# Performance work log

Hardware: AMD Instinct MI355X
Metric: run time of the kernel (lower is better)

Reference implementation:

```python
import jax, jax.numpy as jnp
import numpy as np


def setup_inputs() -> dict:
    key = jax.random.key(0)
    k1, k2 = jax.random.split(key)
    B, D, N = 8, 3, 8192
    preds = jax.random.normal(k1, (B, D, N), dtype=jnp.float32)
    gts = jax.random.normal(k2, (B, D, N), dtype=jnp.float32)
    return {"preds": preds, "gts": gts}


def _chamfer(preds, gts):
    # preds, gts: [B, 3, N] -> x, y: [B, N, 3]
    x = jnp.swapaxes(preds, 2, 1)
    y = jnp.swapaxes(gts, 2, 1)
    # Squared-norm rows/cols + cross term: P[b,i,j] = |x_i|^2 + |y_j|^2 - 2 x_i.y_j
    rx = jnp.sum(x * x, axis=-1)              # [B, Nx]
    ry = jnp.sum(y * y, axis=-1)              # [B, Ny]
    zz = jnp.einsum("bnd,bmd->bnm", x, y)     # [B, Nx, Ny]
    P = rx[:, :, None] + ry[:, None, :] - 2.0 * zz
    loss_1 = jnp.sum(jnp.min(P, axis=1))      # nearest pred for each gt
    loss_2 = jnp.sum(jnp.min(P, axis=2))      # nearest gt for each pred
    return loss_1 + loss_2


def reference(preds, gts):
    return _chamfer(preds, gts)
```

## Files before the change

kernel.cpp:

```cpp
#include <hip/hip_runtime.h>
#include <hip/hip_bf16.h>


typedef float f32x2 __attribute__((ext_vector_type(2)));
typedef float f32x4 __attribute__((ext_vector_type(4)));

#define CN 8192
#define NBATCH 8
#define BQ 2048
#define IPT 8
#define SPLITS 8
#define RB (CN / SPLITS)
#define QCHUNKS (CN / BQ)
#define NPAIR (CN / 2)

__global__ __launch_bounds__(256) void chamfer_pack(
    const float* __restrict__ preds, const float* __restrict__ gts,
    f32x4* __restrict__ xyP, f32x4* __restrict__ zwP,
    f32x4* __restrict__ xyG, f32x4* __restrict__ zwG,
    double* __restrict__ acc, unsigned* __restrict__ cnt) {
  const int g = blockIdx.x * 256 + threadIdx.x;
  if (g == 0) { *acc = 0.0; *cnt = 0u; }
  const int tt  = g >> 15;
  const int idx = g & 32767;
  const int b = idx >> 12, j = idx & (NPAIR - 1);
  const float* __restrict__ src = (tt ? gts : preds) + b * 3 * CN;
  const float2 vx = ((const float2*)(src))[j];
  const float2 vy = ((const float2*)(src + CN))[j];
  const float2 vz = ((const float2*)(src + 2 * CN))[j];
  const float w0 = -0.5f * fmaf(vx.x, vx.x, fmaf(vy.x, vy.x, vz.x * vz.x));
  const float w1 = -0.5f * fmaf(vx.y, vx.y, fmaf(vy.y, vy.y, vz.y * vz.y));
  f32x4* __restrict__ xy = tt ? xyG : xyP;
  f32x4* __restrict__ zw = tt ? zwG : zwP;
  xy[b * NPAIR + j] = (f32x4){vx.x, vx.y, vy.x, vy.y};
  zw[b * NPAIR + j] = (f32x4){vz.x, vz.y, w0, w1};
}

__global__ __launch_bounds__(256, 2) void chamfer_partial(
    const float* __restrict__ preds, const float* __restrict__ gts,
    const f32x4* __restrict__ xyP, const f32x4* __restrict__ zwP,
    const f32x4* __restrict__ xyG, const f32x4* __restrict__ zwG,
    float* __restrict__ partial) {
  const int bid = blockIdx.x;
  const int s     = bid & (SPLITS - 1);
  const int qc    = (bid >> 3) & (QCHUNKS - 1);
  const int batch = (bid >> 5) & (NBATCH - 1);
  const int dir   = bid >> 8;

  const float* __restrict__ Q = (dir ? gts : preds) + batch * 3 * CN;
  const f32x4* __restrict__ XY =
      (dir ? xyP : xyG) + batch * NPAIR + s * (RB / 2);
  const f32x4* __restrict__ ZW =
      (dir ? zwP : zwG) + batch * NPAIR + s * (RB / 2);
  const int tid = threadIdx.x;

  __shared__ f32x4 lxy[RB / 2];
  __shared__ f32x4 lzw[RB / 2];
  lxy[tid]       = XY[tid];
  lxy[tid + 256] = XY[tid + 256];
  lzw[tid]       = ZW[tid];
  lzw[tid + 256] = ZW[tid + 256];

  f32x2 bx[IPT], by[IPT], bz[IPT];
  float xw[IPT], mm[IPT];
#pragma unroll
  for (int k = 0; k < IPT; ++k) {
    const int q = qc * BQ + k * 256 + tid;
    const float a0 = Q[q], a1 = Q[CN + q], a2 = Q[2 * CN + q];
    bx[k] = (f32x2){a0, a0};
    by[k] = (f32x2){a1, a1};
    bz[k] = (f32x2){a2, a2};
    xw[k] = -0.5f * fmaf(a0, a0, fmaf(a1, a1, a2 * a2));
    mm[k] = -INFINITY;
  }
  __syncthreads();

#pragma unroll 4
  for (int p = 0; p < RB / 2; ++p) {
    const f32x4 xy = lxy[p];
    const f32x4 zw = lzw[p];
    const f32x2 X2 = xy.lo, Y2 = xy.hi, Z2 = zw.lo, W2 = zw.hi;
#pragma unroll
    for (int k = 0; k < IPT; ++k) {
      f32x2 t;
      asm("v_pk_fma_f32 %0, %1, %2, %3"
          : "=v"(t) : "v"(bz[k]), "v"(Z2), "v"(W2));
      asm("v_pk_fma_f32 %0, %1, %2, %0"
          : "+v"(t) : "v"(by[k]), "v"(Y2));
      asm("v_pk_fma_f32 %0, %1, %2, %0"
          : "+v"(t) : "v"(bx[k]), "v"(X2));
      asm("v_max3_f32 %0, %0, %1, %2"
          : "+v"(mm[k]) : "v"(t.x), "v"(t.y));
    }
  }

  float* __restrict__ P =
      partial +
      (size_t)(((dir * NBATCH + batch) * QCHUNKS + qc) * SPLITS + s) * BQ;
#pragma unroll
  for (int k = 0; k < IPT; ++k) P[k * 256 + tid] = -2.0f * (xw[k] + mm[k]);
}

__global__ __launch_bounds__(256) void chamfer_reduce(
    const float* __restrict__ partial, double* __restrict__ acc,
    unsigned* __restrict__ cnt, float* __restrict__ out) {
  const int tid = threadIdx.x;
  const int g = blockIdx.x * 256 + tid;
  const int qlocal = g & (BQ - 1);
  const int grp = g >> 11;

  const float* __restrict__ P = partial + (size_t)grp * (SPLITS * BQ) + qlocal;
  float m = P[0];
#pragma unroll
  for (int s2 = 1; s2 < SPLITS; ++s2) m = fminf(m, P[s2 * BQ]);

  float v = m;
#pragma unroll
  for (int off = 32; off > 0; off >>= 1) v += __shfl_down(v, off, 64);

  __shared__ float wsum[4];
  if ((tid & 63) == 0) wsum[tid >> 6] = v;
  __syncthreads();
  if (tid == 0) {
    atomicAdd(acc, (double)(wsum[0] + wsum[1] + wsum[2] + wsum[3]));
    __threadfence();
    const unsigned t = atomicAdd(cnt, 1u);
    if (t == gridDim.x - 1) {
      const double total = atomicAdd(acc, 0.0);
      out[0] = (float)total;
    }
  }
}

extern "C" void kernel_launch(void* const* d_in, const int* in_sizes, int n_in,
                              void* d_out, int out_size, void* d_ws, size_t ws_size,
                              hipStream_t stream) {
  const float* preds = (const float*)d_in[0];
  const float* gts   = (const float*)d_in[1];

  double*   acc = (double*)d_ws;
  unsigned* cnt = (unsigned*)((char*)d_ws + 8);
  char* base = (char*)d_ws + 256;
  const size_t PAIRB = (size_t)NBATCH * NPAIR * 16;
  f32x4* xyP = (f32x4*)(base);
  f32x4* zwP = (f32x4*)(base + PAIRB);
  f32x4* xyG = (f32x4*)(base + 2 * PAIRB);
  f32x4* zwG = (f32x4*)(base + 3 * PAIRB);
  float* partial = (float*)(base + 4 * PAIRB);

  chamfer_pack<<<256, 256, 0, stream>>>(preds, gts, xyP, zwP, xyG, zwG, acc, cnt);
  chamfer_partial<<<512, 256, 0, stream>>>(preds, gts, xyP, zwP, xyG, zwG, partial);
  chamfer_reduce<<<512, 256, 0, stream>>>(partial, acc, cnt, (float*)d_out);
}
```

Measured before the change: 155.4 us.

## Fuse point packing into partial kernel and retile to 16 queries per thread

Drops the separate pack kernel: each block now loads its reference slice straight from the inputs, computes the packed xy/zw and norm terms, and stores them in LDS. The accumulator reset moves to a small hipMemsetAsync. Tiling changes to 4096-query chunks, 16 queries per thread and 16 reference splits, and the LDS reads are software-pipelined one iteration ahead. This removes a kernel launch and a global round trip, at the cost of higher register pressure with IPT=16 and losing the occupancy hint in launch_bounds.

Result: no change. 153.2 us (-1.4%).

```diff
diff --git a/kernel.cpp b/kernel.cpp
--- a/kernel.cpp
+++ b/kernel.cpp
@@ -7,59 +7,38 @@
 
 #define CN 8192
 #define NBATCH 8
-#define BQ 2048
-#define IPT 8
-#define SPLITS 8
+#define BQ 4096
+#define IPT 16
+#define SPLITS 16
 #define RB (CN / SPLITS)
+#define NP (RB / 2)
 #define QCHUNKS (CN / BQ)
-#define NPAIR (CN / 2)
 
-__global__ __launch_bounds__(256) void chamfer_pack(
+__global__ __launch_bounds__(256) void chamfer_partial(
     const float* __restrict__ preds, const float* __restrict__ gts,
-    f32x4* __restrict__ xyP, f32x4* __restrict__ zwP,
-    f32x4* __restrict__ xyG, f32x4* __restrict__ zwG,
-    double* __restrict__ acc, unsigned* __restrict__ cnt) {
-  const int g = blockIdx.x * 256 + threadIdx.x;
-  if (g == 0) { *acc = 0.0; *cnt = 0u; }
-  const int tt  = g >> 15;
-  const int idx = g & 32767;
-  const int b = idx >> 12, j = idx & (NPAIR - 1);
-  const float* __restrict__ src = (tt ? gts : preds) + b * 3 * CN;
-  const float2 vx = ((const float2*)(src))[j];
-  const float2 vy = ((const float2*)(src + CN))[j];
-  const float2 vz = ((const float2*)(src + 2 * CN))[j];
-  const float w0 = -0.5f * fmaf(vx.x, vx.x, fmaf(vy.x, vy.x, vz.x * vz.x));
-  const float w1 = -0.5f * fmaf(vx.y, vx.y, fmaf(vy.y, vy.y, vz.y * vz.y));
-  f32x4* __restrict__ xy = tt ? xyG : xyP;
-  f32x4* __restrict__ zw = tt ? zwG : zwP;
-  xy[b * NPAIR + j] = (f32x4){vx.x, vx.y, vy.x, vy.y};
-  zw[b * NPAIR + j] = (f32x4){vz.x, vz.y, w0, w1};
-}
-
-__global__ __launch_bounds__(256, 2) void chamfer_partial(
-    const float* __restrict__ preds, const float* __restrict__ gts,
-    const f32x4* __restrict__ xyP, const f32x4* __restrict__ zwP,
-    const f32x4* __restrict__ xyG, const f32x4* __restrict__ zwG,
     float* __restrict__ partial) {
   const int bid = blockIdx.x;
   const int s     = bid & (SPLITS - 1);
-  const int qc    = (bid >> 3) & (QCHUNKS - 1);
+  const int qc    = (bid >> 4) & (QCHUNKS - 1);
   const int batch = (bid >> 5) & (NBATCH - 1);
   const int dir   = bid >> 8;
 
   const float* __restrict__ Q = (dir ? gts : preds) + batch * 3 * CN;
-  const f32x4* __restrict__ XY =
-      (dir ? xyP : xyG) + batch * NPAIR + s * (RB / 2);
-  const f32x4* __restrict__ ZW =
-      (dir ? zwP : zwG) + batch * NPAIR + s * (RB / 2);
+  const float* __restrict__ R = (dir ? preds : gts) + batch * 3 * CN;
   const int tid = threadIdx.x;
 
-  __shared__ f32x4 lxy[RB / 2];
-  __shared__ f32x4 lzw[RB / 2];
-  lxy[tid]       = XY[tid];
-  lxy[tid + 256] = XY[tid + 256];
-  lzw[tid]       = ZW[tid];
-  lzw[tid + 256] = ZW[tid + 256];
+  __shared__ f32x4 lxy[NP];
+  __shared__ f32x4 lzw[NP];
+  {
+    const int j = s * NP + tid;
+    const float2 vx = ((const float2*)R)[j];
+    const float2 vy = ((const float2*)(R + CN))[j];
+    const float2 vz = ((const float2*)(R + 2 * CN))[j];
+    const float w0 = -0.5f * fmaf(vx.x, vx.x, fmaf(vy.x, vy.x, vz.x * vz.x));
+    const float w1 = -0.5f * fmaf(vx.y, vx.y, fmaf(vy.y, vy.y, vz.y * vz.y));
+    lxy[tid] = (f32x4){vx.x, vx.y, vy.x, vy.y};
+    lzw[tid] = (f32x4){vz.x, vz.y, w0, w1};
+  }
 
   f32x2 bx[IPT], by[IPT], bz[IPT];
   float xw[IPT], mm[IPT];
@@ -75,10 +54,11 @@
   }
   __syncthreads();
 
-#pragma unroll 4
-  for (int p = 0; p < RB / 2; ++p) {
-    const f32x4 xy = lxy[p];
-    const f32x4 zw = lzw[p];
+  f32x4 xy = lxy[0], zw = lzw[0];
+#pragma unroll 2
+  for (int p = 0; p < NP; ++p) {
+    const f32x4 nxy = lxy[(p + 1) & (NP - 1)];
+    const f32x4 nzw = lzw[(p + 1) & (NP - 1)];
     const f32x2 X2 = xy.lo, Y2 = xy.hi, Z2 = zw.lo, W2 = zw.hi;
 #pragma unroll
     for (int k = 0; k < IPT; ++k) {
@@ -92,6 +72,7 @@
       asm("v_max3_f32 %0, %0, %1, %2"
           : "+v"(mm[k]) : "v"(t.x), "v"(t.y));
     }
+    xy = nxy; zw = nzw;
   }
 
   float* __restrict__ P =
@@ -107,7 +88,7 @@
   const int tid = threadIdx.x;
   const int g = blockIdx.x * 256 + tid;
   const int qlocal = g & (BQ - 1);
-  const int grp = g >> 11;
+  const int grp = g >> 12;
 
   const float* __restrict__ P = partial + (size_t)grp * (SPLITS * BQ) + qlocal;
   float m = P[0];
@@ -138,17 +119,11 @@
   const float* preds = (const float*)d_in[0];
   const float* gts   = (const float*)d_in[1];
 
-  double*   acc = (double*)d_ws;
-  unsigned* cnt = (unsigned*)((char*)d_ws + 8);
-  char* base = (char*)d_ws + 256;
-  const size_t PAIRB = (size_t)NBATCH * NPAIR * 16;
-  f32x4* xyP = (f32x4*)(base);
-  f32x4* zwP = (f32x4*)(base + PAIRB);
-  f32x4* xyG = (f32x4*)(base + 2 * PAIRB);
-  f32x4* zwG = (f32x4*)(base + 3 * PAIRB);
-  float* partial = (float*)(base + 4 * PAIRB);
+  double*   acc     = (double*)d_ws;
+  unsigned* cnt     = (unsigned*)((char*)d_ws + 8);
+  float*    partial = (float*)((char*)d_ws + 256);
 
-  chamfer_pack<<<256, 256, 0, stream>>>(preds, gts, xyP, zwP, xyG, zwG, acc, cnt);
-  chamfer_partial<<<512, 256, 0, stream>>>(preds, gts, xyP, zwP, xyG, zwG, partial);
+  hipMemsetAsync(d_ws, 0, 12, stream);
+  chamfer_partial<<<512, 256, 0, stream>>>(preds, gts, partial);
   chamfer_reduce<<<512, 256, 0, stream>>>(partial, acc, cnt, (float*)d_out);
 }
```
